# Kernel optimization log

Measured on AMD Instinct MI355X. Metric: run time of the kernel, lower is better.

Reference implementation:

```python
import jax, jax.numpy as jnp
import numpy as np

N_NODES = 50000
N_EDGES = 800000
D_IN = 256
D_HID = 128
NUM_LAYERS = 6
ALPHA = 0.1
THETA = 0.5
EPS = 1e-5  # BatchNorm1d default eps


def setup_inputs() -> dict:
    key = jax.random.key(0)
    ks = jax.random.split(key, 6)
    x = jax.random.normal(ks[0], (N_NODES, D_IN), dtype=jnp.float32)
    edge_index = jax.random.randint(ks[1], (2, N_EDGES), 0, N_NODES)
    # GCNConv(D_IN, D_HID): weight + bias
    W_lin = jax.random.normal(ks[2], (D_IN, D_HID), dtype=jnp.float32) / np.sqrt(D_IN).astype(np.float32)
    b_lin = jnp.zeros((D_HID,), jnp.float32)
    # GCN2Conv weight1 per layer (shared_weights=True -> only weight1, no bias)
    W1s = jax.random.normal(ks[3], (NUM_LAYERS - 1, D_HID, D_HID), dtype=jnp.float32) / np.sqrt(D_HID).astype(np.float32)
    # BatchNorm1d affine params per intermediate layer
    bn_gamma = jnp.ones((NUM_LAYERS - 2, D_HID), jnp.float32)
    bn_beta = jnp.zeros((NUM_LAYERS - 2, D_HID), jnp.float32)
    return {"x": x, "edge_index": edge_index, "W_lin": W_lin, "b_lin": b_lin,
            "W1s": W1s, "bn_gamma": bn_gamma, "bn_beta": bn_beta}


def _gcn_conv(x, W, b, edge_index):
    # PyG GCNConv: transform, add self-loops, D^{-1/2}(A+I)D^{-1/2} aggregation.
    n = x.shape[0]
    xw = x @ W  # [N, D_HID]
    loop = jnp.arange(n)
    src = jnp.concatenate([edge_index[0], loop])
    dst = jnp.concatenate([edge_index[1], loop])
    deg = jax.ops.segment_sum(jnp.ones(src.shape, xw.dtype), dst, num_segments=n)
    dinv = jax.lax.rsqrt(jnp.maximum(deg, 1.0))  # deg >= 1 thanks to self loops
    w = dinv[src] * dinv[dst]  # [E+N]
    return jax.ops.segment_sum(xw[src] * w[:, None], dst, num_segments=n) + b


def _gcn2_conv(z, x0, W1, edge_index, beta):
    # GCN2Conv with normalize=False, shared_weights=True:
    # h = (1-alpha)*sum_{j->i} z_j + alpha*x0 ; out = (1-beta)*h + beta*(h @ W1)
    n = z.shape[0]
    agg = jax.ops.segment_sum(z[edge_index[0]], edge_index[1], num_segments=n)
    h = (1.0 - ALPHA) * agg + ALPHA * x0
    return (1.0 - beta) * h + beta * (h @ W1)


def _batchnorm(z, gamma, beta_p):
    # training-mode BatchNorm1d over the node dimension (biased variance)
    mu = jnp.mean(z, axis=0)
    var = jnp.var(z, axis=0)
    return (z - mu) * jax.lax.rsqrt(var + EPS) * gamma + beta_p


def reference(x, edge_index, W_lin, b_lin, W1s, bn_gamma, bn_beta):
    z = _gcn_conv(x, W_lin, b_lin, edge_index)
    x0 = z
    n_convs = NUM_LAYERS - 1
    # GCN2Conv layer index l = i+1 -> beta_l = log(theta/l + 1)
    betas = [float(np.log(THETA / (i + 1) + 1.0)) for i in range(n_convs)]
    for i in range(n_convs):  # dropout=0.0 -> identity, omitted
        z = _gcn2_conv(z, x0, W1s[i], edge_index, betas[i])
        if i < n_convs - 1:
            z = _batchnorm(z, bn_gamma[i], bn_beta[i])
            z = jax.nn.relu(z)
    return z
```

## Files before the change

kernel.cpp:

```cpp
#include <hip/hip_runtime.h>
#include <math.h>

#define N_NODES 50000
#define N_EDGES 800000
#define D_IN 256
#define D_HID 128
#define ALPHA 0.1f
#define EPS 1e-5f

#define NBUCK 391
#define EPB 4096
#define NBLK 196

typedef __attribute__((ext_vector_type(8))) short bf16x8;
typedef __attribute__((ext_vector_type(4))) float f32x4;

static __device__ __forceinline__ unsigned short f2bf(float f) {
    unsigned int x = __float_as_uint(f);
    return (unsigned short)((x + 0x7fffu + ((x >> 16) & 1u)) >> 16);
}
static __device__ __forceinline__ float blo(unsigned int v) {
    return __uint_as_float(v << 16);
}
static __device__ __forceinline__ float bhi(unsigned int v) {
    return __uint_as_float(v & 0xffff0000u);
}
static __device__ __forceinline__ void unpack8(uint4 u, float* f) {
    f[0] = blo(u.x); f[1] = bhi(u.x);
    f[2] = blo(u.y); f[3] = bhi(u.y);
    f[4] = blo(u.z); f[5] = bhi(u.z);
    f[6] = blo(u.w); f[7] = bhi(u.w);
}

__global__ __launch_bounds__(256) void k_hist(const int* __restrict__ dst,
                                              int* __restrict__ hist, int e) {
    __shared__ int h[NBUCK];
    int t = threadIdx.x;
    for (int i = t; i < NBUCK; i += 256) h[i] = 0;
    __syncthreads();
    int base = blockIdx.x * EPB;
    int lim = e - base;
    if (lim > EPB) lim = EPB;
    for (int i = t; i < lim; i += 256) atomicAdd(&h[dst[base + i] >> 7], 1);
    __syncthreads();
    for (int i = t; i < NBUCK; i += 256) hist[blockIdx.x * NBUCK + i] = h[i];
}

__global__ __launch_bounds__(256) void k_bkscan(const int* __restrict__ hist,
                                                int* __restrict__ offsT, int* __restrict__ btot) {
    __shared__ int sh[256];
    int b = blockIdx.x;
    int t = threadIdx.x;
    int v = (t < NBLK) ? hist[t * NBUCK + b] : 0;
    sh[t] = v;
    __syncthreads();
    for (int ofs = 1; ofs < 256; ofs <<= 1) {
        int y = (t >= ofs) ? sh[t - ofs] : 0;
        __syncthreads();
        sh[t] += y;
        __syncthreads();
    }
    if (t < NBLK) offsT[b * NBLK + t] = sh[t] - v;
    if (t == 255) btot[b] = sh[255];
}

__global__ __launch_bounds__(512) void k_bbase(const int* __restrict__ btot,
                                               int* __restrict__ bbase, int* __restrict__ rp) {
    __shared__ int sh[512];
    int t = threadIdx.x;
    int v = (t < NBUCK) ? btot[t] : 0;
    sh[t] = v;
    __syncthreads();
    for (int ofs = 1; ofs < 512; ofs <<= 1) {
        int y = (t >= ofs) ? sh[t - ofs] : 0;
        __syncthreads();
        sh[t] += y;
        __syncthreads();
    }
    if (t < NBUCK) bbase[t] = sh[t] - v;
    if (t == 0) rp[N_NODES] = N_EDGES;
}

__global__ __launch_bounds__(256) void k_scatter(const int* __restrict__ src,
                                                 const int* __restrict__ dst,
                                                 const int* __restrict__ offsT,
                                                 const int* __restrict__ bbase,
                                                 unsigned int* __restrict__ buck, int e) {
    __shared__ int h[NBUCK];
    int t = threadIdx.x;
    for (int i = t; i < NBUCK; i += 256) h[i] = 0;
    __syncthreads();
    int base = blockIdx.x * EPB;
    int lim = e - base;
    if (lim > EPB) lim = EPB;
    for (int i = t; i < lim; i += 256) {
        int d = dst[base + i];
        int s = src[base + i];
        int b = d >> 7;
        int lp = atomicAdd(&h[b], 1);
        int pos = bbase[b] + offsT[b * NBLK + blockIdx.x] + lp;
        buck[pos] = (unsigned int)s | ((unsigned int)(d & 127) << 16);
    }
}

__global__ __launch_bounds__(256) void k_csr(const unsigned int* __restrict__ buck,
                                             const int* __restrict__ bbase,
                                             const int* __restrict__ btot,
                                             int* __restrict__ rp, float* __restrict__ dinv,
                                             unsigned short* __restrict__ cs) {
    __shared__ int dcnt[128];
    __shared__ int doff[128];
    int b = blockIdx.x;
    int t = threadIdx.x;
    if (t < 128) dcnt[t] = 0;
    __syncthreads();
    int base = bbase[b];
    int tot = btot[b];
    for (int i = t; i < tot; i += 256) {
        unsigned int v = buck[base + i];
        atomicAdd(&dcnt[(v >> 16) & 127], 1);
    }
    __syncthreads();
    if (t < 128) doff[t] = dcnt[t];
    __syncthreads();
    for (int ofs = 1; ofs < 128; ofs <<= 1) {
        int y = 0;
        if (t < 128 && t >= ofs) y = doff[t - ofs];
        __syncthreads();
        if (t < 128) doff[t] += y;
        __syncthreads();
    }
    int gd0 = b << 7;
    if (t < 128) {
        int ex = doff[t] - dcnt[t];
        if (gd0 + t < N_NODES) {
            rp[gd0 + t] = base + ex;
            dinv[gd0 + t] = rsqrtf((float)(dcnt[t] + 1));
        }
        dcnt[t] = ex;
    }
    __syncthreads();
    for (int i = t; i < tot; i += 256) {
        unsigned int v = buck[base + i];
        int p = atomicAdd(&dcnt[(v >> 16) & 127], 1);
        cs[base + p] = (unsigned short)(v & 0xffffu);
    }
}

__global__ __launch_bounds__(256) void k_cast_x(const float4* __restrict__ x, ushort2* __restrict__ xb,
                                                int n4) {
    int i = blockIdx.x * 256 + threadIdx.x;
    if (i < n4) {
        float4 v = x[i];
        ushort2 a;
        a.x = f2bf(v.x); a.y = f2bf(v.y);
        ushort2 b;
        b.x = f2bf(v.z); b.y = f2bf(v.w);
        xb[i * 2] = a;
        xb[i * 2 + 1] = b;
    }
}

__global__ __launch_bounds__(256) void k_prep_w(const float* __restrict__ W_lin,
                                                const float* __restrict__ W1s,
                                                unsigned short* __restrict__ Wlt,
                                                unsigned short* __restrict__ Wt) {
    int idx = blockIdx.x * 256 + threadIdx.x;
    if (idx < 128 * 256) {
        int c = idx >> 8, k = idx & 255;
        Wlt[idx] = f2bf(W_lin[k * 128 + c]);
    } else {
        int j = idx - 128 * 256;
        if (j < 5 * 128 * 128) {
            int l = j >> 14;
            int rem = j & 16383;
            int c = rem >> 7, k = rem & 127;
            float bet = logf(0.5f / (float)(l + 1) + 1.0f);
            float v = bet * W1s[l * 16384 + k * 128 + c];
            if (c == k) v += 1.0f - bet;
            Wt[j] = f2bf(v);
        }
    }
}

template <int K>
__global__ __launch_bounds__(256) void k_mgemm(const unsigned short* __restrict__ A,
                                               const unsigned short* __restrict__ Bt,
                                               unsigned short* __restrict__ outb, int M) {
    __shared__ short lds[2 * 128 * 136];
    short* As = lds;
    short* Bs = lds + 128 * 136;

    int t = threadIdx.x;
    int lane = t & 63;
    int wave = t >> 6;
    int wr = wave >> 1, wc = wave & 1;
    int row0 = blockIdx.x * 128;

    f32x4 acc[4][4];
#pragma unroll
    for (int m = 0; m < 4; ++m)
#pragma unroll
        for (int n = 0; n < 4; ++n) acc[m][n] = (f32x4){0.f, 0.f, 0.f, 0.f};

    int sr = t >> 1;
    int sh = t & 1;

    for (int k0 = 0; k0 < K; k0 += 128) {
        {
            int gr = row0 + sr;
            uint4 zero = {0, 0, 0, 0};
            const uint4* gp = (const uint4*)(A + (size_t)gr * K + k0 + sh * 64);
#pragma unroll
            for (int u = 0; u < 8; ++u) {
                uint4 v = (gr < M) ? gp[u] : zero;
                *(uint4*)(As + sr * 136 + sh * 64 + u * 8) = v;
            }
        }
        {
            const uint4* gp = (const uint4*)(Bt + (size_t)sr * K + k0 + sh * 64);
#pragma unroll
            for (int u = 0; u < 8; ++u) {
                *(uint4*)(Bs + sr * 136 + sh * 64 + u * 8) = gp[u];
            }
        }
        __syncthreads();

#pragma unroll
        for (int ks = 0; ks < 4; ++ks) {
            bf16x8 af[4], bfr[4];
#pragma unroll
            for (int m = 0; m < 4; ++m)
                af[m] = *(const bf16x8*)(As + (wr * 64 + m * 16 + (lane & 15)) * 136 + ks * 32 + (lane >> 4) * 8);
#pragma unroll
            for (int n = 0; n < 4; ++n)
                bfr[n] = *(const bf16x8*)(Bs + (wc * 64 + n * 16 + (lane & 15)) * 136 + ks * 32 + (lane >> 4) * 8);
#pragma unroll
            for (int m = 0; m < 4; ++m)
#pragma unroll
                for (int n = 0; n < 4; ++n)
                    acc[m][n] = __builtin_amdgcn_mfma_f32_16x16x32_bf16(af[m], bfr[n], acc[m][n], 0, 0, 0);
        }
        __syncthreads();
    }

    short* Z = lds;
#pragma unroll
    for (int m = 0; m < 4; ++m)
#pragma unroll
        for (int n = 0; n < 4; ++n)
#pragma unroll
            for (int r = 0; r < 4; ++r) {
                int rl = wr * 64 + m * 16 + (lane >> 4) * 4 + r;
                int cl = wc * 64 + n * 16 + (lane & 15);
                Z[rl * 136 + cl] = (short)f2bf(acc[m][n][r]);
            }
    __syncthreads();
    int gr = row0 + sr;
    if (gr < M) {
#pragma unroll
        for (int u = 0; u < 8; ++u)
            *(uint4*)(outb + (size_t)gr * 128 + sh * 64 + u * 8) = *(uint4*)(Z + sr * 136 + sh * 64 + u * 8);
    }
}

template <int MODE>
__global__ __launch_bounds__(256) void k_lgemm(const unsigned short* __restrict__ A,
                                               const unsigned short* __restrict__ Bt,
                                               unsigned short* __restrict__ outb,
                                               float* __restrict__ outf,
                                               float* __restrict__ bn_s, float* __restrict__ bn_q,
                                               int M) {
    __shared__ short As[128 * 136];
    int t = threadIdx.x;
    int lane = t & 63;
    int wave = t >> 6;
    int wr = wave >> 1, wc = wave & 1;
    int row0 = blockIdx.x * 128;

    bf16x8 bfr[4][4];
#pragma unroll
    for (int ks = 0; ks < 4; ++ks)
#pragma unroll
        for (int n = 0; n < 4; ++n)
            bfr[ks][n] = *(const bf16x8*)(Bt + (size_t)(wc * 64 + n * 16 + (lane & 15)) * 128 + ks * 32 + (lane >> 4) * 8);

    int sr = t >> 1, sh = t & 1;
    {
        int gr = row0 + sr;
        uint4 zero = {0, 0, 0, 0};
        const uint4* gp = (const uint4*)(A + (size_t)gr * 128 + sh * 64);
#pragma unroll
        for (int u = 0; u < 8; ++u) {
            uint4 v = (gr < M) ? gp[u] : zero;
            *(uint4*)(As + sr * 136 + sh * 64 + u * 8) = v;
        }
    }
    __syncthreads();

    f32x4 acc[4][4];
#pragma unroll
    for (int m = 0; m < 4; ++m)
#pragma unroll
        for (int n = 0; n < 4; ++n) acc[m][n] = (f32x4){0.f, 0.f, 0.f, 0.f};

#pragma unroll
    for (int ks = 0; ks < 4; ++ks) {
        bf16x8 af[4];
#pragma unroll
        for (int m = 0; m < 4; ++m)
            af[m] = *(const bf16x8*)(As + (wr * 64 + m * 16 + (lane & 15)) * 136 + ks * 32 + (lane >> 4) * 8);
#pragma unroll
        for (int m = 0; m < 4; ++m)
#pragma unroll
            for (int n = 0; n < 4; ++n)
                acc[m][n] = __builtin_amdgcn_mfma_f32_16x16x32_bf16(af[m], bfr[ks][n], acc[m][n], 0, 0, 0);
    }

    if (MODE == 1) {
        float sum[4] = {0.f, 0.f, 0.f, 0.f}, sq[4] = {0.f, 0.f, 0.f, 0.f};
#pragma unroll
        for (int n = 0; n < 4; ++n)
#pragma unroll
            for (int m = 0; m < 4; ++m)
#pragma unroll
                for (int r = 0; r < 4; ++r) {
                    float v = acc[m][n][r];
                    sum[n] += v;
                    sq[n] += v * v;
                }
#pragma unroll
        for (int n = 0; n < 4; ++n) {
            sum[n] += __shfl_xor(sum[n], 16);
            sum[n] += __shfl_xor(sum[n], 32);
            sq[n] += __shfl_xor(sq[n], 16);
            sq[n] += __shfl_xor(sq[n], 32);
        }
        if (lane < 16) {
#pragma unroll
            for (int n = 0; n < 4; ++n) {
                int col = wc * 64 + n * 16 + lane;
                atomicAdd(&bn_s[col], sum[n]);
                atomicAdd(&bn_q[col], sq[n]);
            }
        }
    }

    if (MODE == 2) {
#pragma unroll
        for (int m = 0; m < 4; ++m)
#pragma unroll
            for (int n = 0; n < 4; ++n)
#pragma unroll
                for (int r = 0; r < 4; ++r) {
                    int gr = row0 + wr * 64 + m * 16 + (lane >> 4) * 4 + r;
                    int cl = wc * 64 + n * 16 + (lane & 15);
                    if (gr < M) outf[(size_t)gr * 128 + cl] = acc[m][n][r];
                }
    } else {
        __syncthreads();
        short* Z = As;
#pragma unroll
        for (int m = 0; m < 4; ++m)
#pragma unroll
            for (int n = 0; n < 4; ++n)
#pragma unroll
                for (int r = 0; r < 4; ++r) {
                    int rl = wr * 64 + m * 16 + (lane >> 4) * 4 + r;
                    int cl = wc * 64 + n * 16 + (lane & 15);
                    Z[rl * 136 + cl] = (short)f2bf(acc[m][n][r]);
                }
        __syncthreads();
        int gr = row0 + sr;
        if (gr < M) {
#pragma unroll
            for (int u = 0; u < 8; ++u)
                *(uint4*)(outb + (size_t)gr * 128 + sh * 64 + u * 8) = *(uint4*)(Z + sr * 136 + sh * 64 + u * 8);
        }
    }
}

template <int MODE>
__global__ __launch_bounds__(128) void k_agg(const uint4* __restrict__ src4,
                                             const uint4* __restrict__ x04,
                                             const int* __restrict__ rp,
                                             const unsigned short* __restrict__ cs,
                                             const float* __restrict__ dinv,
                                             const float* __restrict__ b_lin,
                                             const float* __restrict__ st,
                                             uint4* __restrict__ dst4,
                                             float* __restrict__ bns, int n) {
    if (blockIdx.x == 0) {
        bns[threadIdx.x] = 0.f;
        bns[threadIdx.x + 128] = 0.f;
    }
    int node = blockIdx.x;
    if (node >= n) return;
    int half = threadIdx.x >> 6;
    int lane = threadIdx.x & 63;
    int q = lane >> 3;
    int c = lane & 7;
    int col4 = half * 8 + c;

    int start = __builtin_amdgcn_readfirstlane(rp[node]);
    int end = __builtin_amdgcn_readfirstlane(rp[node + 1]);

    float sc[8], tc[8];
    if (MODE == 2) {
        float4 s0 = ((const float4*)st)[col4 * 2];
        float4 s1 = ((const float4*)st)[col4 * 2 + 1];
        float4 t0 = ((const float4*)st)[32 + col4 * 2];
        float4 t1 = ((const float4*)st)[32 + col4 * 2 + 1];
        sc[0] = s0.x; sc[1] = s0.y; sc[2] = s0.z; sc[3] = s0.w;
        sc[4] = s1.x; sc[5] = s1.y; sc[6] = s1.z; sc[7] = s1.w;
        tc[0] = t0.x; tc[1] = t0.y; tc[2] = t0.z; tc[3] = t0.w;
        tc[4] = t1.x; tc[5] = t1.y; tc[6] = t1.z; tc[7] = t1.w;
    }
    float dn = (MODE == 0) ? dinv[node] : 0.f;

    float acc[8];
#pragma unroll
    for (int i = 0; i < 8; ++i) acc[i] = 0.f;

#define ACCW(vv, ww)                                                       \
    {                                                                      \
        float f_[8];                                                       \
        unpack8(vv, f_);                                                   \
        if (MODE == 2) {                                                   \
            _Pragma("unroll") for (int i_ = 0; i_ < 8; ++i_)               \
                acc[i_] = fmaf(ww, fmaxf(fmaf(sc[i_], f_[i_], tc[i_]), 0.f), acc[i_]); \
        } else {                                                           \
            _Pragma("unroll") for (int i_ = 0; i_ < 8; ++i_)               \
                acc[i_] = fmaf(ww, f_[i_], acc[i_]);                       \
        }                                                                  \
    }
#define ACCP(vv)                                                           \
    {                                                                      \
        float f_[8];                                                       \
        unpack8(vv, f_);                                                   \
        if (MODE == 2) {                                                   \
            _Pragma("unroll") for (int i_ = 0; i_ < 8; ++i_)               \
                acc[i_] += fmaxf(fmaf(sc[i_], f_[i_], tc[i_]), 0.f);       \
        } else {                                                           \
            _Pragma("unroll") for (int i_ = 0; i_ < 8; ++i_)               \
                acc[i_] += f_[i_];                                         \
        }                                                                  \
    }

    for (int base = start; base < end; base += 64) {
        int cnt = end - base;
        if (cnt > 64) cnt = 64;
        int li = (lane < cnt) ? lane : (cnt - 1);
        int myi = (int)cs[base + li];
        float myw = (MODE == 0) ? dinv[myi] : 0.f;

        int j = 0;
        for (; j + 16 <= cnt; j += 16) {
            int j0 = j + q, j1 = j + 8 + q;
            int i0 = __shfl(myi, j0);
            int i1 = __shfl(myi, j1);
            uint4 v0 = src4[(size_t)i0 * 16 + col4];
            uint4 v1 = src4[(size_t)i1 * 16 + col4];
            if (MODE == 0) {
                float w0 = __shfl(myw, j0) * dn;
                float w1 = __shfl(myw, j1) * dn;
                ACCW(v0, w0);
                ACCW(v1, w1);
            } else {
                ACCP(v0);
                ACCP(v1);
            }
        }
        for (; j + 8 <= cnt; j += 8) {
            int j0 = j + q;
            int i0 = __shfl(myi, j0);
            uint4 v0 = src4[(size_t)i0 * 16 + col4];
            if (MODE == 0) {
                float w0 = __shfl(myw, j0) * dn;
                ACCW(v0, w0);
            } else {
                ACCP(v0);
            }
        }
        if (j < cnt) {
            int jj = j + q;
            bool act = jj < cnt;
            int js = act ? jj : (cnt - 1);
            int i0 = __shfl(myi, js);
            uint4 v0 = src4[(size_t)i0 * 16 + col4];
            float m = act ? 1.f : 0.f;
            float w0 = (MODE == 0) ? (__shfl(myw, js) * dn * m) : m;
            ACCW(v0, w0);
        }
    }
#undef ACCW
#undef ACCP

#pragma unroll
    for (int i = 0; i < 8; ++i) {
        acc[i] += __shfl_xor(acc[i], 8);
        acc[i] += __shfl_xor(acc[i], 16);
        acc[i] += __shfl_xor(acc[i], 32);
    }

    if (lane < 8) {
        float res[8];
        if (MODE == 0) {
            uint4 sv = src4[(size_t)node * 16 + col4];
            float fs[8];
            unpack8(sv, fs);
            float w2 = dn * dn;
            float4 b0 = ((const float4*)b_lin)[col4 * 2];
            float4 b1 = ((const float4*)b_lin)[col4 * 2 + 1];
            float bb[8] = {b0.x, b0.y, b0.z, b0.w, b1.x, b1.y, b1.z, b1.w};
#pragma unroll
            for (int i = 0; i < 8; ++i) res[i] = fmaf(w2, fs[i], acc[i]) + bb[i];
        } else {
            uint4 xv = x04[(size_t)node * 16 + col4];
            float fx[8];
            unpack8(xv, fx);
#pragma unroll
            for (int i = 0; i < 8; ++i) res[i] = fmaf(ALPHA, fx[i], (1.0f - ALPHA) * acc[i]);
        }
        uint4 o;
        o.x = (unsigned int)f2bf(res[0]) | ((unsigned int)f2bf(res[1]) << 16);
        o.y = (unsigned int)f2bf(res[2]) | ((unsigned int)f2bf(res[3]) << 16);
        o.z = (unsigned int)f2bf(res[4]) | ((unsigned int)f2bf(res[5]) << 16);
        o.w = (unsigned int)f2bf(res[6]) | ((unsigned int)f2bf(res[7]) << 16);
        dst4[(size_t)node * 16 + col4] = o;
    }
}

__global__ void k_bn_fin(const float* __restrict__ bn_s, const float* __restrict__ bn_q,
                         const float* __restrict__ gamma, const float* __restrict__ betap,
                         float* __restrict__ st, int n) {
    int c = threadIdx.x;
    float inv_n = 1.0f / (float)n;
    float mu = bn_s[c] * inv_n;
    float var = bn_q[c] * inv_n - mu * mu;
    var = fmaxf(var, 0.f);
    float s = gamma[c] * rsqrtf(var + EPS);
    st[c] = s;
    st[128 + c] = betap[c] - mu * s;
}

extern "C" void kernel_launch(void* const* d_in, const int* in_sizes, int n_in,
                              void* d_out, int out_size, void* d_ws, size_t ws_size,
                              hipStream_t stream) {
    const float* x = (const float*)d_in[0];
    const int* ei = (const int*)d_in[1];
    const float* W_lin = (const float*)d_in[2];
    const float* b_lin = (const float*)d_in[3];
    const float* W1s = (const float*)d_in[4];
    const float* gam = (const float*)d_in[5];
    const float* betp = (const float*)d_in[6];
    float* out = (float*)d_out;

    char* ws = (char*)d_ws;
    size_t off = 0;
    auto alloc = [&](size_t b) { size_t p = off; off = (off + b + 255) & ~(size_t)255; return p; };
    int* rp = (int*)(ws + alloc((size_t)(N_NODES + 1) * 4));
    unsigned short* cs = (unsigned short*)(ws + alloc((size_t)N_EDGES * 2));
    float* dinv = (float*)(ws + alloc((size_t)N_NODES * 4));
    int* hist = (int*)(ws + alloc((size_t)NBLK * NBUCK * 4));
    int* offsT = (int*)(ws + alloc((size_t)NBUCK * NBLK * 4));
    int* btot = (int*)(ws + alloc((size_t)NBUCK * 4));
    int* bbase = (int*)(ws + alloc((size_t)NBUCK * 4));
    unsigned int* buck = (unsigned int*)(ws + alloc((size_t)N_EDGES * 4));
    unsigned short* xb = (unsigned short*)(ws + alloc((size_t)N_NODES * D_IN * 2));
    unsigned short* xwb = (unsigned short*)(ws + alloc((size_t)N_NODES * D_HID * 2));
    unsigned short* x0b = (unsigned short*)(ws + alloc((size_t)N_NODES * D_HID * 2));
    unsigned short* zb = (unsigned short*)(ws + alloc((size_t)N_NODES * D_HID * 2));
    unsigned short* hb = (unsigned short*)(ws + alloc((size_t)N_NODES * D_HID * 2));
    unsigned short* Wlt = (unsigned short*)(ws + alloc((size_t)128 * 256 * 2));
    unsigned short* Wt = (unsigned short*)(ws + alloc((size_t)5 * 128 * 128 * 2));
    float* bns = (float*)(ws + alloc(256 * 4));
    float* st = (float*)(ws + alloc(256 * 4));

    const int ggrid = (N_NODES + 127) / 128;
    const int agrid = N_NODES;

    k_hist<<<NBLK, 256, 0, stream>>>(ei + N_EDGES, hist, N_EDGES);
    k_bkscan<<<NBUCK, 256, 0, stream>>>(hist, offsT, btot);
    k_bbase<<<1, 512, 0, stream>>>(btot, bbase, rp);
    k_scatter<<<NBLK, 256, 0, stream>>>(ei, ei + N_EDGES, offsT, bbase, buck, N_EDGES);
    k_csr<<<NBUCK, 256, 0, stream>>>(buck, bbase, btot, rp, dinv, cs);

    k_cast_x<<<(N_NODES * D_IN / 4 + 255) / 256, 256, 0, stream>>>((const float4*)x, (ushort2*)xb,
                                                                   N_NODES * D_IN / 4);
    k_prep_w<<<(128 * 256 + 5 * 128 * 128 + 255) / 256, 256, 0, stream>>>(W_lin, W1s, Wlt, Wt);

    k_mgemm<D_IN><<<ggrid, 256, 0, stream>>>(xb, Wlt, xwb, N_NODES);
    k_agg<0><<<agrid, 128, 0, stream>>>((const uint4*)xwb, nullptr, rp, cs, dinv, b_lin,
                                        nullptr, (uint4*)x0b, bns, N_NODES);

    for (int i = 0; i < 5; ++i) {
        const unsigned short* zsrc = (i == 0) ? x0b : zb;
        if (i == 0)
            k_agg<1><<<agrid, 128, 0, stream>>>((const uint4*)zsrc, (const uint4*)x0b,
                                                rp, cs, nullptr, nullptr, nullptr,
                                                (uint4*)hb, bns, N_NODES);
        else
            k_agg<2><<<agrid, 128, 0, stream>>>((const uint4*)zsrc, (const uint4*)x0b,
                                                rp, cs, nullptr, nullptr, st,
                                                (uint4*)hb, bns, N_NODES);
        const unsigned short* W1 = Wt + (size_t)i * 128 * 128;
        if (i < 4) {
            k_lgemm<1><<<ggrid, 256, 0, stream>>>(hb, W1, zb, nullptr, bns, bns + 128, N_NODES);
            k_bn_fin<<<1, 128, 0, stream>>>(bns, bns + 128, gam + (size_t)i * 128,
                                            betp + (size_t)i * 128, st, N_NODES);
        } else {
            k_lgemm<2><<<ggrid, 256, 0, stream>>>(hb, W1, nullptr, out, nullptr, nullptr, N_NODES);
        }
    }
}
```

Measured before the change: 448.4 us.

## Store hidden features in column-sliced layout and aggregate per slice

Node feature buffers change from row-major [N,128] bf16 to 8 column slices of 16 features each ([8][N][16]). The aggregation kernel now runs one wave per (node, slice) with 32 edges in flight per wave, and the GEMM kernels read and write the sliced layout. Each slice of the gathered data is 1.6MB, so the random neighbour gathers should stay resident in cache while all blocks for that slice run. The cost is 8x more aggregation waves, repeated CSR index reads per slice, and an extra shuffle-reduction stage.

```diff
diff --git a/kernel.cpp b/kernel.cpp
--- a/kernel.cpp
+++ b/kernel.cpp
@@ -186,7 +186,7 @@
 template <int K>
 __global__ __launch_bounds__(256) void k_mgemm(const unsigned short* __restrict__ A,
                                                const unsigned short* __restrict__ Bt,
-                                               unsigned short* __restrict__ outb, int M) {
+                                               uint4* __restrict__ outp, int M) {
     __shared__ short lds[2 * 128 * 136];
     short* As = lds;
     short* Bs = lds + 128 * 136;
@@ -256,18 +256,19 @@
                 Z[rl * 136 + cl] = (short)f2bf(acc[m][n][r]);
             }
     __syncthreads();
-    int gr = row0 + sr;
+    int rr = t >> 1, cc = t & 1;
+    int gr = row0 + rr;
     if (gr < M) {
 #pragma unroll
-        for (int u = 0; u < 8; ++u)
-            *(uint4*)(outb + (size_t)gr * 128 + sh * 64 + u * 8) = *(uint4*)(Z + sr * 136 + sh * 64 + u * 8);
+        for (int p = 0; p < 8; ++p)
+            outp[((size_t)p * M + gr) * 2 + cc] = *(uint4*)(Z + rr * 136 + p * 16 + cc * 8);
     }
 }
 
 template <int MODE>
-__global__ __launch_bounds__(256) void k_lgemm(const unsigned short* __restrict__ A,
+__global__ __launch_bounds__(256) void k_lgemm(const uint4* __restrict__ Ap,
                                                const unsigned short* __restrict__ Bt,
-                                               unsigned short* __restrict__ outb,
+                                               uint4* __restrict__ outp,
                                                float* __restrict__ outf,
                                                float* __restrict__ bn_s, float* __restrict__ bn_q,
                                                int M) {
@@ -285,15 +286,14 @@
         for (int n = 0; n < 4; ++n)
             bfr[ks][n] = *(const bf16x8*)(Bt + (size_t)(wc * 64 + n * 16 + (lane & 15)) * 128 + ks * 32 + (lane >> 4) * 8);
 
-    int sr = t >> 1, sh = t & 1;
     {
-        int gr = row0 + sr;
+        int rr = t >> 1, cc = t & 1;
+        int gr = row0 + rr;
         uint4 zero = {0, 0, 0, 0};
-        const uint4* gp = (const uint4*)(A + (size_t)gr * 128 + sh * 64);
-#pragma unroll
-        for (int u = 0; u < 8; ++u) {
-            uint4 v = (gr < M) ? gp[u] : zero;
-            *(uint4*)(As + sr * 136 + sh * 64 + u * 8) = v;
+#pragma unroll
+        for (int p = 0; p < 8; ++p) {
+            uint4 v = (gr < M) ? Ap[((size_t)p * M + gr) * 2 + cc] : zero;
+            *(uint4*)(As + rr * 136 + p * 16 + cc * 8) = v;
         }
     }
     __syncthreads();
@@ -371,52 +371,51 @@
                     Z[rl * 136 + cl] = (short)f2bf(acc[m][n][r]);
                 }
         __syncthreads();
-        int gr = row0 + sr;
+        int rr = t >> 1, cc = t & 1;
+        int gr = row0 + rr;
         if (gr < M) {
 #pragma unroll
-            for (int u = 0; u < 8; ++u)
-                *(uint4*)(outb + (size_t)gr * 128 + sh * 64 + u * 8) = *(uint4*)(Z + sr * 136 + sh * 64 + u * 8);
+            for (int p = 0; p < 8; ++p)
+                outp[((size_t)p * M + gr) * 2 + cc] = *(uint4*)(Z + rr * 136 + p * 16 + cc * 8);
         }
     }
 }
 
 template <int MODE>
-__global__ __launch_bounds__(128) void k_agg(const uint4* __restrict__ src4,
-                                             const uint4* __restrict__ x04,
+__global__ __launch_bounds__(256) void k_agg(const uint4* __restrict__ srcp,
+                                             const uint4* __restrict__ x0p,
                                              const int* __restrict__ rp,
                                              const unsigned short* __restrict__ cs,
                                              const float* __restrict__ dinv,
                                              const float* __restrict__ b_lin,
                                              const float* __restrict__ st,
-                                             uint4* __restrict__ dst4,
+                                             uint4* __restrict__ dstp,
                                              float* __restrict__ bns, int n) {
-    if (blockIdx.x == 0) {
-        bns[threadIdx.x] = 0.f;
-        bns[threadIdx.x + 128] = 0.f;
-    }
-    int node = blockIdx.x;
+    if (blockIdx.x == 0) bns[threadIdx.x] = 0.f;
+
+    int slice = blockIdx.x & 7;
+    int node = (blockIdx.x >> 3) * 4 + (threadIdx.x >> 6);
     if (node >= n) return;
-    int half = threadIdx.x >> 6;
     int lane = threadIdx.x & 63;
-    int q = lane >> 3;
-    int c = lane & 7;
-    int col4 = half * 8 + c;
+    int q = lane >> 1;
+    int c = lane & 1;
 
     int start = __builtin_amdgcn_readfirstlane(rp[node]);
     int end = __builtin_amdgcn_readfirstlane(rp[node + 1]);
 
     float sc[8], tc[8];
     if (MODE == 2) {
-        float4 s0 = ((const float4*)st)[col4 * 2];
-        float4 s1 = ((const float4*)st)[col4 * 2 + 1];
-        float4 t0 = ((const float4*)st)[32 + col4 * 2];
-        float4 t1 = ((const float4*)st)[32 + col4 * 2 + 1];
+        float4 s0 = ((const float4*)st)[slice * 4 + c * 2];
+        float4 s1 = ((const float4*)st)[slice * 4 + c * 2 + 1];
+        float4 t0 = ((const float4*)st)[32 + slice * 4 + c * 2];
+        float4 t1 = ((const float4*)st)[32 + slice * 4 + c * 2 + 1];
         sc[0] = s0.x; sc[1] = s0.y; sc[2] = s0.z; sc[3] = s0.w;
         sc[4] = s1.x; sc[5] = s1.y; sc[6] = s1.z; sc[7] = s1.w;
         tc[0] = t0.x; tc[1] = t0.y; tc[2] = t0.z; tc[3] = t0.w;
         tc[4] = t1.x; tc[5] = t1.y; tc[6] = t1.z; tc[7] = t1.w;
     }
     float dn = (MODE == 0) ? dinv[node] : 0.f;
+    size_t pbase = (size_t)slice * n;
 
     float acc[8];
 #pragma unroll
@@ -454,43 +453,26 @@
         int myi = (int)cs[base + li];
         float myw = (MODE == 0) ? dinv[myi] : 0.f;
 
-        int j = 0;
-        for (; j + 16 <= cnt; j += 16) {
-            int j0 = j + q, j1 = j + 8 + q;
-            int i0 = __shfl(myi, j0);
-            int i1 = __shfl(myi, j1);
-            uint4 v0 = src4[(size_t)i0 * 16 + col4];
-            uint4 v1 = src4[(size_t)i1 * 16 + col4];
-            if (MODE == 0) {
-                float w0 = __shfl(myw, j0) * dn;
-                float w1 = __shfl(myw, j1) * dn;
-                ACCW(v0, w0);
-                ACCW(v1, w1);
+        for (int j = 0; j < cnt; j += 32) {
+            int jj = j + q;
+            if (j + 32 <= cnt) {
+                int i0 = __shfl(myi, jj);
+                uint4 v = srcp[(pbase + i0) * 2 + c];
+                if (MODE == 0) {
+                    float w = __shfl(myw, jj) * dn;
+                    ACCW(v, w);
+                } else {
+                    ACCP(v);
+                }
             } else {
-                ACCP(v0);
-                ACCP(v1);
+                bool act = jj < cnt;
+                int js = act ? jj : (cnt - 1);
+                int i0 = __shfl(myi, js);
+                uint4 v = srcp[(pbase + i0) * 2 + c];
+                float m = act ? 1.f : 0.f;
+                float w = (MODE == 0) ? (__shfl(myw, js) * dn * m) : m;
+                ACCW(v, w);
             }
-        }
-        for (; j + 8 <= cnt; j += 8) {
-            int j0 = j + q;
-            int i0 = __shfl(myi, j0);
-            uint4 v0 = src4[(size_t)i0 * 16 + col4];
-            if (MODE == 0) {
-                float w0 = __shfl(myw, j0) * dn;
-                ACCW(v0, w0);
-            } else {
-                ACCP(v0);
-            }
-        }
-        if (j < cnt) {
-            int jj = j + q;
-            bool act = jj < cnt;
-            int js = act ? jj : (cnt - 1);
-            int i0 = __shfl(myi, js);
-            uint4 v0 = src4[(size_t)i0 * 16 + col4];
-            float m = act ? 1.f : 0.f;
-            float w0 = (MODE == 0) ? (__shfl(myw, js) * dn * m) : m;
-            ACCW(v0, w0);
         }
     }
 #undef ACCW
@@ -498,25 +480,27 @@
 
 #pragma unroll
     for (int i = 0; i < 8; ++i) {
+        acc[i] += __shfl_xor(acc[i], 2);
+        acc[i] += __shfl_xor(acc[i], 4);
         acc[i] += __shfl_xor(acc[i], 8);
         acc[i] += __shfl_xor(acc[i], 16);
         acc[i] += __shfl_xor(acc[i], 32);
     }
 
-    if (lane < 8) {
+    if (lane < 2) {
         float res[8];
         if (MODE == 0) {
-            uint4 sv = src4[(size_t)node * 16 + col4];
+            uint4 sv = srcp[(pbase + node) * 2 + c];
             float fs[8];
             unpack8(sv, fs);
             float w2 = dn * dn;
-            float4 b0 = ((const float4*)b_lin)[col4 * 2];
-            float4 b1 = ((const float4*)b_lin)[col4 * 2 + 1];
+            float4 b0 = ((const float4*)b_lin)[slice * 4 + c * 2];
+            float4 b1 = ((const float4*)b_lin)[slice * 4 + c * 2 + 1];
             float bb[8] = {b0.x, b0.y, b0.z, b0.w, b1.x, b1.y, b1.z, b1.w};
 #pragma unroll
             for (int i = 0; i < 8; ++i) res[i] = fmaf(w2, fs[i], acc[i]) + bb[i];
         } else {
-            uint4 xv = x04[(size_t)node * 16 + col4];
+            uint4 xv = x0p[(pbase + node) * 2 + c];
             float fx[8];
             unpack8(xv, fx);
 #pragma unroll
@@ -527,7 +511,7 @@
         o.y = (unsigned int)f2bf(res[2]) | ((unsigned int)f2bf(res[3]) << 16);
         o.z = (unsigned int)f2bf(res[4]) | ((unsigned int)f2bf(res[5]) << 16);
         o.w = (unsigned int)f2bf(res[6]) | ((unsigned int)f2bf(res[7]) << 16);
-        dst4[(size_t)node * 16 + col4] = o;
+        dstp[(pbase + node) * 2 + c] = o;
     }
 }
 
@@ -568,17 +552,17 @@
     int* bbase = (int*)(ws + alloc((size_t)NBUCK * 4));
     unsigned int* buck = (unsigned int*)(ws + alloc((size_t)N_EDGES * 4));
     unsigned short* xb = (unsigned short*)(ws + alloc((size_t)N_NODES * D_IN * 2));
-    unsigned short* xwb = (unsigned short*)(ws + alloc((size_t)N_NODES * D_HID * 2));
-    unsigned short* x0b = (unsigned short*)(ws + alloc((size_t)N_NODES * D_HID * 2));
-    unsigned short* zb = (unsigned short*)(ws + alloc((size_t)N_NODES * D_HID * 2));
-    unsigned short* hb = (unsigned short*)(ws + alloc((size_t)N_NODES * D_HID * 2));
+    uint4* xwp = (uint4*)(ws + alloc((size_t)N_NODES * D_HID * 2));
+    uint4* x0p = (uint4*)(ws + alloc((size_t)N_NODES * D_HID * 2));
+    uint4* zp = (uint4*)(ws + alloc((size_t)N_NODES * D_HID * 2));
+    uint4* hp = (uint4*)(ws + alloc((size_t)N_NODES * D_HID * 2));
     unsigned short* Wlt = (unsigned short*)(ws + alloc((size_t)128 * 256 * 2));
     unsigned short* Wt = (unsigned short*)(ws + alloc((size_t)5 * 128 * 128 * 2));
     float* bns = (float*)(ws + alloc(256 * 4));
     float* st = (float*)(ws + alloc(256 * 4));
 
     const int ggrid = (N_NODES + 127) / 128;
-    const int agrid = N_NODES;
+    const int agrid = ((N_NODES + 3) / 4) * 8;
 
     k_hist<<<NBLK, 256, 0, stream>>>(ei + N_EDGES, hist, N_EDGES);
     k_bkscan<<<NBUCK, 256, 0, stream>>>(hist, offsT, btot);
@@ -590,27 +574,25 @@
                                                                    N_NODES * D_IN / 4);
     k_prep_w<<<(128 * 256 + 5 * 128 * 128 + 255) / 256, 256, 0, stream>>>(W_lin, W1s, Wlt, Wt);
 
-    k_mgemm<D_IN><<<ggrid, 256, 0, stream>>>(xb, Wlt, xwb, N_NODES);
-    k_agg<0><<<agrid, 128, 0, stream>>>((const uint4*)xwb, nullptr, rp, cs, dinv, b_lin,
-                                        nullptr, (uint4*)x0b, bns, N_NODES);
+    k_mgemm<D_IN><<<ggrid, 256, 0, stream>>>(xb, Wlt, xwp, N_NODES);
+    k_agg<0><<<agrid, 256, 0, stream>>>(xwp, nullptr, rp, cs, dinv, b_lin,
+                                        nullptr, x0p, bns, N_NODES);
 
     for (int i = 0; i < 5; ++i) {
-        const unsigned short* zsrc = (i == 0) ? x0b : zb;
+        const uint4* zsrc = (i == 0) ? x0p : zp;
         if (i == 0)
-            k_agg<1><<<agrid, 128, 0, stream>>>((const uint4*)zsrc, (const uint4*)x0b,
-                                                rp, cs, nullptr, nullptr, nullptr,
-                                                (uint4*)hb, bns, N_NODES);
+            k_agg<1><<<agrid, 256, 0, stream>>>(zsrc, x0p, rp, cs, nullptr, nullptr, nullptr,
+                                                hp, bns, N_NODES);
         else
-            k_agg<2><<<agrid, 128, 0, stream>>>((const uint4*)zsrc, (const uint4*)x0b,
-                                                rp, cs, nullptr, nullptr, st,
-                                                (uint4*)hb, bns, N_NODES);
+            k_agg<2><<<agrid, 256, 0, stream>>>(zsrc, x0p, rp, cs, nullptr, nullptr, st,
+                                                hp, bns, N_NODES);
         const unsigned short* W1 = Wt + (size_t)i * 128 * 128;
         if (i < 4) {
-            k_lgemm<1><<<ggrid, 256, 0, stream>>>(hb, W1, zb, nullptr, bns, bns + 128, N_NODES);
+            k_lgemm<1><<<ggrid, 256, 0, stream>>>(hp, W1, zp, nullptr, bns, bns + 128, N_NODES);
             k_bn_fin<<<1, 128, 0, stream>>>(bns, bns + 128, gam + (size_t)i * 128,
                                             betp + (size_t)i * 128, st, N_NODES);
         } else {
-            k_lgemm<2><<<ggrid, 256, 0, stream>>>(hb, W1, nullptr, out, nullptr, nullptr, N_NODES);
-        }
-    }
-}
+            k_lgemm<2><<<ggrid, 256, 0, stream>>>(hp, W1, nullptr, out, nullptr, nullptr, N_NODES);
+        }
+    }
+}
```

New measurement: 1.196 ms. 2.67x slower.
